# Optimization experiments

Hardware: AMD Instinct MI355X
Metric: run time of the kernel (lower is better)

## Reference

```python
import jax, jax.numpy as jnp
import numpy as np

N_NODES = 100000
N_EDGES = 1700000  # 1.6M random edges + 100k self-loops (dgl.add_self_loop)
HID = 128
N_GRAPHS = 64
N_CLASSES = 10
T_STEPS = 5


def setup_inputs() -> dict:
    key = jax.random.key(0)
    ks = jax.random.split(key, 12)
    m = jax.random.normal(ks[0], (N_NODES,), dtype=jnp.float32)
    n_rand = N_EDGES - N_NODES
    src_r = jax.random.randint(ks[1], (n_rand,), 0, N_NODES)
    dst_r = jax.random.randint(ks[2], (n_rand,), 0, N_NODES)
    loops = jnp.arange(N_NODES)
    src = jnp.concatenate([src_r, loops])
    dst = jnp.concatenate([dst_r, loops])
    graph_ids = jnp.sort(jax.random.randint(ks[3], (N_NODES,), 0, N_GRAPHS))
    s = 0.05
    W_e = jax.random.normal(ks[4], (HID, HID), dtype=jnp.float32) * s
    b_e = jnp.zeros((HID,), dtype=jnp.float32)
    W_ih = jax.random.normal(ks[5], (3 * HID, HID), dtype=jnp.float32) * s
    b_ih = jnp.zeros((3 * HID,), dtype=jnp.float32)
    W_hh = jax.random.normal(ks[6], (3 * HID, HID), dtype=jnp.float32) * s
    b_hh = jnp.zeros((3 * HID,), dtype=jnp.float32)
    W_cls = jax.random.normal(ks[7], (N_CLASSES, HID), dtype=jnp.float32) * s
    b_cls = jnp.zeros((N_CLASSES,), dtype=jnp.float32)
    return {"m": m, "W_e": W_e, "b_e": b_e, "W_ih": W_ih, "b_ih": b_ih,
            "W_hh": W_hh, "b_hh": b_hh, "W_cls": W_cls, "b_cls": b_cls,
            "src": src, "dst": dst, "graph_ids": graph_ids, "n_graphs": N_GRAPHS}


def _gated_graph_forward(m, W_e, b_e, W_ih, b_ih, W_hh, b_hh, W_cls, b_cls,
                         src, dst, graph_ids, n_graphs):
    n_nodes = m.shape[0]
    hid = W_e.shape[0]
    # h = ndata['m'].view(-1,1), zero-padded to out_feats (DGL GatedGraphConv)
    h = jnp.zeros((n_nodes, hid), dtype=m.dtype).at[:, 0].set(m)
    for _ in range(T_STEPS):
        # single edge type: a[v] = sum_{(u,v) in E} W_e h[u] + b_e
        msg = (h @ W_e.T + b_e)[src]                       # [E, H]
        a = jax.ops.segment_sum(msg, dst, num_segments=n_nodes)
        # torch.nn.GRUCell(a, h); gate order: r, z, n
        gi = a @ W_ih.T + b_ih
        gh = h @ W_hh.T + b_hh
        i_r, i_z, i_n = jnp.split(gi, 3, axis=-1)
        h_r, h_z, h_n = jnp.split(gh, 3, axis=-1)
        r = jax.nn.sigmoid(i_r + h_r)
        z = jax.nn.sigmoid(i_z + h_z)
        n = jnp.tanh(i_n + r * h_n)
        h = (1.0 - z) * n + z * h
    h = jax.nn.relu(h)
    # dgl.mean_nodes: per-graph mean over nodes
    sums = jax.ops.segment_sum(h, graph_ids, num_segments=n_graphs)
    cnt = jax.ops.segment_sum(jnp.ones((n_nodes,), h.dtype), graph_ids,
                              num_segments=n_graphs)
    hg = sums / jnp.maximum(cnt, 1.0)[:, None]             # [G, H]
    return hg @ W_cls.T + b_cls                            # [G, C]


def reference(m, W_e, b_e, W_ih, b_ih, W_hh, b_hh, W_cls, b_cls,
              src, dst, graph_ids, n_graphs):
    return _gated_graph_forward(m, W_e, b_e, W_ih, b_ih, W_hh, b_hh,
                                W_cls, b_cls, src, dst, graph_ids, n_graphs)
```

## Files before the change

### kernel.cpp

```cpp
#include <hip/hip_runtime.h>

#define HID 128
#define G3  384
#define TSTEPS 5
#define BSHIFT 9
#define BNODES (1 << BSHIFT)
#define MAXBUK 256
#define PART_EPB 8192

typedef unsigned int  uint;
typedef unsigned short ushort;

typedef float  f32x4  __attribute__((ext_vector_type(4)));
typedef __bf16 bf16x8 __attribute__((ext_vector_type(8)));

union B8u { uint4 u; bf16x8 b; ushort s[8]; };

static __device__ inline ushort f2bf(float f) {
  uint u = __float_as_uint(f);
  uint r = u + 0x7fffu + ((u >> 16) & 1u);
  return (ushort)(r >> 16);
}
static __device__ inline float bf2f(ushort s) {
  return __uint_as_float(((uint)s) << 16);
}

__global__ __launch_bounds__(128) void k_weights(
    const float* __restrict__ W_e, const float* __restrict__ b_e,
    const float* __restrict__ W_ih, const float* __restrict__ W_hh,
    ushort* __restrict__ Wcomb, ushort* __restrict__ Whh16, float* __restrict__ bvec,
    ushort* __restrict__ Wc0, ushort* __restrict__ Wh0)
{
  int j = blockIdx.x, t = threadIdx.x;
  if (j < G3) {
    __shared__ float row[HID];
    row[t] = W_ih[j * HID + t];
    __syncthreads();
    float acc = 0.f;
    for (int k = 0; k < HID; ++k) acc = fmaf(row[k], W_e[k * HID + t], acc);
    Wcomb[j * HID + t] = f2bf(acc);
    if (t == 0) {
      Wc0[j] = f2bf(acc);
      float b = 0.f;
      for (int k = 0; k < HID; ++k) b += row[k] * b_e[k];
      bvec[j] = b;
    }
  } else {
    int j2 = j - G3;
    Whh16[j2 * HID + t] = f2bf(W_hh[j2 * HID + t]);
    if (t == 0) Wh0[j2] = f2bf(W_hh[j2 * HID]);
  }
}

__global__ __launch_bounds__(256) void k_bh(const int* __restrict__ dst,
                                            int* __restrict__ bhist, int E) {
  __shared__ int lh[MAXBUK];
  int t = threadIdx.x;
  if (t < MAXBUK) lh[t] = 0;
  __syncthreads();
  for (int e = blockIdx.x * 256 + t; e < E; e += gridDim.x * 256)
    atomicAdd(&lh[dst[e] >> BSHIFT], 1);
  __syncthreads();
  if (t < MAXBUK && lh[t]) atomicAdd(&bhist[t], lh[t]);
}

__global__ __launch_bounds__(256) void k_bsc(const int* __restrict__ bhist,
                                             int* __restrict__ bbase,
                                             int* __restrict__ gcur,
                                             int* __restrict__ rowptr, int E, int N) {
  __shared__ int ls[MAXBUK];
  int t = threadIdx.x;
  ls[t] = bhist[t];
  __syncthreads();
  if (t == 0) {
    int run = 0;
    for (int i = 0; i < MAXBUK; ++i) {
      bbase[i] = run; gcur[i] = run; run += ls[i];
    }
    bbase[MAXBUK] = run;
    rowptr[N] = E;
  }
}

__global__ __launch_bounds__(256) void k_part(
    const int* __restrict__ src, const int* __restrict__ dst,
    int* __restrict__ gcur, uint* __restrict__ ebuf, int E) {
  __shared__ int lh[MAXBUK], lbase[MAXBUK], lcur[MAXBUK];
  int t = threadIdx.x;
  int base = blockIdx.x * PART_EPB;
  if (t < MAXBUK) lh[t] = 0;
  __syncthreads();
#pragma unroll 4
  for (int j = 0; j < PART_EPB / 256; ++j) {
    int e = base + j * 256 + t;
    if (e < E) atomicAdd(&lh[dst[e] >> BSHIFT], 1);
  }
  __syncthreads();
  if (t < MAXBUK) {
    lbase[t] = lh[t] ? atomicAdd(&gcur[t], lh[t]) : 0;
    lcur[t] = 0;
  }
  __syncthreads();
#pragma unroll 4
  for (int j = 0; j < PART_EPB / 256; ++j) {
    int e = base + j * 256 + t;
    if (e < E) {
      int d = dst[e];
      int b = d >> BSHIFT;
      int p = atomicAdd(&lcur[b], 1);
      ebuf[lbase[b] + p] = (uint)src[e] | ((uint)(d & (BNODES - 1)) << 20);
    }
  }
}

__global__ __launch_bounds__(256) void k_fill2(
    const uint* __restrict__ ebuf, const int* __restrict__ bbase,
    int* __restrict__ csrc, int* __restrict__ rowptr, int* __restrict__ deg, int N) {
  __shared__ int hcnt[BNODES];
  __shared__ int wls[4];
  int t = threadIdx.x;
  int b = blockIdx.x;
  int ebeg = bbase[b], eend = bbase[b + 1];
  for (int i = t; i < BNODES; i += 256) hcnt[i] = 0;
  __syncthreads();
  for (int e = ebeg + t; e < eend; e += 256)
    atomicAdd(&hcnt[ebuf[e] >> 20], 1);
  __syncthreads();
  const int PER = BNODES / 256;
  int lane = t & 63, wv = t >> 6;
  int x[PER]; int s = 0;
#pragma unroll
  for (int i = 0; i < PER; ++i) { x[i] = hcnt[PER * t + i]; s += x[i]; }
  int incl = s;
#pragma unroll
  for (int off = 1; off < 64; off <<= 1) {
    int u = __shfl_up(incl, off, 64);
    if (lane >= off) incl += u;
  }
  if (lane == 63) wls[wv] = incl;
  __syncthreads();
  int wbase = 0;
  for (int i = 0; i < wv; ++i) wbase += wls[i];
  int run = wbase + incl - s;
#pragma unroll
  for (int i = 0; i < PER; ++i) {
    int node = (b << BSHIFT) + PER * t + i;
    hcnt[PER * t + i] = run;
    if (node < N) { rowptr[node] = ebeg + run; deg[node] = x[i]; }
    run += x[i];
  }
  __syncthreads();
  for (int e = ebeg + t; e < eend; e += 256) {
    uint v = ebuf[e];
    int p = atomicAdd(&hcnt[v >> 20], 1);
    csrc[ebeg + p] = (int)(v & 0xFFFFFu);
  }
}

__global__ void k_minit(const float* __restrict__ m, ushort* __restrict__ m16, int N) {
  int v = blockIdx.x * 256 + threadIdx.x;
  if (v < N) m16[v] = f2bf(m[v]);
}

__global__ __launch_bounds__(256) void k_gather0(
    const int* __restrict__ rowptr, const int* __restrict__ csrc,
    const ushort* __restrict__ m16, ushort* __restrict__ hsum0, int N)
{
  int v = blockIdx.x * 256 + threadIdx.x;
  if (v >= N) return;
  int beg = rowptr[v], end = rowptr[v + 1];
  float a0 = 0.f, a1 = 0.f, a2 = 0.f, a3 = 0.f;
  int e = beg;
  for (; e + 16 <= end; e += 16) {
    a0 += (bf2f(m16[csrc[e + 0]]) + bf2f(m16[csrc[e + 4]])) +
          (bf2f(m16[csrc[e + 8]]) + bf2f(m16[csrc[e + 12]]));
    a1 += (bf2f(m16[csrc[e + 1]]) + bf2f(m16[csrc[e + 5]])) +
          (bf2f(m16[csrc[e + 9]]) + bf2f(m16[csrc[e + 13]]));
    a2 += (bf2f(m16[csrc[e + 2]]) + bf2f(m16[csrc[e + 6]])) +
          (bf2f(m16[csrc[e + 10]]) + bf2f(m16[csrc[e + 14]]));
    a3 += (bf2f(m16[csrc[e + 3]]) + bf2f(m16[csrc[e + 7]])) +
          (bf2f(m16[csrc[e + 11]]) + bf2f(m16[csrc[e + 15]]));
  }
  for (; e < end; e += 4) {
    if (e + 0 < end) a0 += bf2f(m16[csrc[e + 0]]);
    if (e + 1 < end) a1 += bf2f(m16[csrc[e + 1]]);
    if (e + 2 < end) a2 += bf2f(m16[csrc[e + 2]]);
    if (e + 3 < end) a3 += bf2f(m16[csrc[e + 3]]);
  }
  hsum0[v] = f2bf((a0 + a1) + (a2 + a3));
}

__global__ __launch_bounds__(256) void k_gru0(
    const ushort* __restrict__ hsum0, const ushort* __restrict__ m16,
    const int* __restrict__ deg,
    const ushort* __restrict__ Wc0, const ushort* __restrict__ Wh0,
    const float* __restrict__ bvec, const float* __restrict__ b_ih,
    const float* __restrict__ b_hh, ushort* __restrict__ hbn, int N)
{
  int idx = blockIdx.x * 256 + threadIdx.x;
  if (idx >= N * HID) return;
  int n = idx >> 7, d = idx & (HID - 1);
  float s0 = bf2f(hsum0[n]);
  float h0 = bf2f(m16[n]);
  float degf = (float)deg[n];
  float acc0 = s0 * bf2f(Wc0[d]);
  float acc1 = s0 * bf2f(Wc0[d + 128]);
  float acc2 = s0 * bf2f(Wc0[d + 256]);
  float acc3 = h0 * bf2f(Wh0[d]);
  float acc4 = h0 * bf2f(Wh0[d + 128]);
  float acc5 = h0 * bf2f(Wh0[d + 256]);
  float hold = (d == 0) ? h0 : 0.f;
  float ir = acc0 + degf * bvec[d] + b_ih[d];
  float iz = acc1 + degf * bvec[d + 128] + b_ih[d + 128];
  float in_ = acc2 + degf * bvec[d + 256] + b_ih[d + 256];
  float hr = acc3 + b_hh[d];
  float hz = acc4 + b_hh[d + 128];
  float hn = acc5 + b_hh[d + 256];
  float r = __builtin_amdgcn_rcpf(1.f + __expf(-(ir + hr)));
  float z = __builtin_amdgcn_rcpf(1.f + __expf(-(iz + hz)));
  float x2 = in_ + r * hn;
  float e2 = __expf(2.f * x2);
  float nv = 1.f - 2.f * __builtin_amdgcn_rcpf(e2 + 1.f);
  float hv = (1.f - z) * nv + z * hold;
  hbn[idx] = f2bf(hv);
}

__global__ __launch_bounds__(256) void k_gather(
    const int* __restrict__ rowptr, const int* __restrict__ csrc,
    const ushort* __restrict__ hb, ushort* __restrict__ hs16, int N, int nstrip)
{
  int x = blockIdx.x & 7;
  int ii = blockIdx.x >> 3;
  int s = 8 * (ii >> 2) + x;
  if (s >= nstrip) return;
  int v = s * 16 + (ii & 3) * 4 + (threadIdx.x >> 6);
  if (v >= N) return;
  int lane = threadIdx.x & 63;
  int g = lane >> 4;
  int i = lane & 15;
  int beg = rowptr[v], end = rowptr[v + 1];
  float acc[8] = {0.f, 0.f, 0.f, 0.f, 0.f, 0.f, 0.f, 0.f};
  int e = beg;
  for (; e + 16 <= end; e += 16) {
    int s0 = csrc[e + g];
    int s1 = csrc[e + 4 + g];
    int s2 = csrc[e + 8 + g];
    int s3 = csrc[e + 12 + g];
    B8u w0; w0.u = *(const uint4*)(hb + (size_t)s0 * HID + i * 8);
    B8u w1; w1.u = *(const uint4*)(hb + (size_t)s1 * HID + i * 8);
    B8u w2; w2.u = *(const uint4*)(hb + (size_t)s2 * HID + i * 8);
    B8u w3; w3.u = *(const uint4*)(hb + (size_t)s3 * HID + i * 8);
#pragma unroll
    for (int j = 0; j < 8; ++j)
      acc[j] += (bf2f(w0.s[j]) + bf2f(w1.s[j])) + (bf2f(w2.s[j]) + bf2f(w3.s[j]));
  }
  for (; e < end; e += 4) {
    int ee = e + g;
    if (ee < end) {
      int s0 = csrc[ee];
      B8u w; w.u = *(const uint4*)(hb + (size_t)s0 * HID + i * 8);
#pragma unroll
      for (int j = 0; j < 8; ++j) acc[j] += bf2f(w.s[j]);
    }
  }
#pragma unroll
  for (int j = 0; j < 8; ++j) {
    acc[j] += __shfl_xor(acc[j], 16, 64);
    acc[j] += __shfl_xor(acc[j], 32, 64);
  }
  if (g == 0) {
    uint4 ov;
    ov.x = ((uint)f2bf(acc[1]) << 16) | (uint)f2bf(acc[0]);
    ov.y = ((uint)f2bf(acc[3]) << 16) | (uint)f2bf(acc[2]);
    ov.z = ((uint)f2bf(acc[5]) << 16) | (uint)f2bf(acc[4]);
    ov.w = ((uint)f2bf(acc[7]) << 16) | (uint)f2bf(acc[6]);
    *(uint4*)(hs16 + (size_t)v * HID + i * 8) = ov;
  }
}

struct GruCtx2 {
  const ushort* Amat;
  const ushort* hbc; ushort* hbn; const int* deg;
  int l16, quad, gm3, d0, ecol, erow0;
  float bir, biz, bin_, bhr, bhz, bhn, vr, vz, vn;
};

static __device__ __forceinline__ void gru2_loadA(const GruCtx2& c, int s, B8u a[4]) {
  size_t arow = (size_t)(s * 16 + c.l16) * HID + c.quad * 8;
#pragma unroll
  for (int kc = 0; kc < 4; ++kc)
    a[kc].u = *(const uint4*)(c.Amat + arow + kc * 32);
}

static __device__ __forceinline__ void gru2_loadE(const GruCtx2& c, int s,
                                                  float hold[2], float dg[2]) {
  int n0 = s << 4;
  hold[0] = bf2f(c.hbc[(size_t)(n0 + c.erow0) * HID + c.ecol]);
  hold[1] = bf2f(c.hbc[(size_t)(n0 + c.erow0 + 8) * HID + c.ecol]);
  dg[0] = (float)c.deg[n0 + c.erow0];
  dg[1] = (float)c.deg[n0 + c.erow0 + 8];
}

static __device__ __forceinline__ void gru2_step(
    const GruCtx2& c, int s, const B8u a[4], const float hold[2], const float dg[2],
    const B8u bfr[3][4], float (*S)[16][132]) {
  f32x4 acc[3] = {};
#pragma unroll
  for (int kc = 0; kc < 4; ++kc)
#pragma unroll
    for (int g = 0; g < 3; ++g)
      acc[g] = __builtin_amdgcn_mfma_f32_16x16x32_bf16(a[kc].b, bfr[g][kc].b, acc[g], 0, 0, 0);
  __builtin_amdgcn_s_barrier();
#pragma unroll
  for (int g = 0; g < 3; ++g)
#pragma unroll
    for (int rg = 0; rg < 4; ++rg)
      S[c.gm3 + g][c.quad * 4 + rg][c.d0 + c.l16] = acc[g][rg];
  asm volatile("s_waitcnt lgkmcnt(0)" ::: "memory");
  __builtin_amdgcn_sched_barrier(0);
  __builtin_amdgcn_s_barrier();
  int n0 = s << 4;
#pragma unroll
  for (int k = 0; k < 2; ++k) {
    int row = c.erow0 + 8 * k;
    float ir  = S[0][row][c.ecol] + dg[k] * c.vr + c.bir;
    float iz  = S[1][row][c.ecol] + dg[k] * c.vz + c.biz;
    float in_ = S[2][row][c.ecol] + dg[k] * c.vn + c.bin_;
    float hr  = S[3][row][c.ecol] + c.bhr;
    float hz  = S[4][row][c.ecol] + c.bhz;
    float hn  = S[5][row][c.ecol] + c.bhn;
    float r = __builtin_amdgcn_rcpf(1.f + __expf(-(ir + hr)));
    float z = __builtin_amdgcn_rcpf(1.f + __expf(-(iz + hz)));
    float x2 = in_ + r * hn;
    float e2 = __expf(2.f * x2);
    float nv = 1.f - 2.f * __builtin_amdgcn_rcpf(e2 + 1.f);
    float hv = (1.f - z) * nv + z * hold[k];
    c.hbn[(size_t)(n0 + row) * HID + c.ecol] = f2bf(hv);
  }
}

__global__ __launch_bounds__(1024, 4) void k_gru(
    const ushort* __restrict__ hs16,
    const ushort* __restrict__ hbc, ushort* __restrict__ hbn,
    const ushort* __restrict__ Wcomb, const ushort* __restrict__ Whh16,
    const float* __restrict__ bvec, const float* __restrict__ b_ih,
    const float* __restrict__ b_hh, const int* __restrict__ deg, int N)
{
  __shared__ float S[6][16][132];
  const int tid = threadIdx.x;
  const int w = tid >> 6;
  const int lane = tid & 63;
  const int quad = lane >> 4, l16 = lane & 15;
  const int gm = w >> 3;
  const int gw = w & 7;
  const int d0 = gw * 16;

  const ushort* Wmat = gm ? Whh16 : Wcomb;

  B8u bfr[3][4];
#pragma unroll
  for (int g = 0; g < 3; ++g)
#pragma unroll
    for (int kc = 0; kc < 4; ++kc) {
      int j = (d0 + g * 128 + l16) * HID + kc * 32 + quad * 8;
      bfr[g][kc].u = *(const uint4*)(Wmat + j);
    }

  GruCtx2 c;
  c.Amat = gm ? hbc : hs16;
  c.hbc = hbc; c.hbn = hbn; c.deg = deg;
  c.l16 = l16; c.quad = quad; c.gm3 = gm * 3; c.d0 = d0;
  c.ecol = tid & 127;
  c.erow0 = tid >> 7;
  c.bir = b_ih[c.ecol]; c.biz = b_ih[c.ecol + 128]; c.bin_ = b_ih[c.ecol + 256];
  c.bhr = b_hh[c.ecol]; c.bhz = b_hh[c.ecol + 128]; c.bhn = b_hh[c.ecol + 256];
  c.vr = bvec[c.ecol]; c.vz = bvec[c.ecol + 128]; c.vn = bvec[c.ecol + 256];

  const int nstrip = N >> 4;
  const int G = (int)gridDim.x;
  int s = blockIdx.x;
  if (s >= nstrip) return;

  B8u aA[4], aB[4];
  float hA[2], dA[2], hB[2], dB[2];
  gru2_loadA(c, s, aA); gru2_loadE(c, s, hA, dA);

  while (true) {
    int ns = s + G;
    bool more = ns < nstrip;
    if (more) { gru2_loadA(c, ns, aB); gru2_loadE(c, ns, hB, dB); }
    gru2_step(c, s, aA, hA, dA, bfr, S);
    if (!more) break;
    s = ns;
    ns = s + G;
    more = ns < nstrip;
    if (more) { gru2_loadA(c, ns, aA); gru2_loadE(c, ns, hA, dA); }
    gru2_step(c, s, aB, hB, dB, bfr, S);
    if (!more) break;
    s = ns;
  }
}

__global__ __launch_bounds__(64) void k_bounds(const int* __restrict__ gid,
                                               int* __restrict__ cnt, int N, int G) {
  int g = threadIdx.x;
  if (g >= G) return;
  int lo = 0, hi = N;
  while (lo < hi) { int mid = (lo + hi) >> 1; if (gid[mid] < g) lo = mid + 1; else hi = mid; }
  int lb0 = lo;
  lo = 0; hi = N;
  int g1 = g + 1;
  while (lo < hi) { int mid = (lo + hi) >> 1; if (gid[mid] < g1) lo = mid + 1; else hi = mid; }
  cnt[g] = lo - lb0;
}

#define POOL_CHUNK 96
__global__ __launch_bounds__(128) void k_pool(const ushort* __restrict__ hb,
                                              const int* __restrict__ gid,
                                              float* __restrict__ hg, int N) {
  int d = threadIdx.x;
  int start = blockIdx.x * POOL_CHUNK;
  if (start >= N) return;
  int end = min(start + POOL_CHUNK, N);
  float acc = 0.f;
  int g = gid[start];
  for (int n = start; n < end; ++n) {
    int gn = gid[n];
    if (gn != g) { unsafeAtomicAdd(&hg[g * HID + d], acc); acc = 0.f; g = gn; }
    acc += fmaxf(bf2f(hb[(size_t)n * HID + d]), 0.f);
  }
  unsafeAtomicAdd(&hg[g * HID + d], acc);
}

__global__ __launch_bounds__(640) void k_cls(const float* __restrict__ hg,
                                             const int* __restrict__ cnt,
                                             const float* __restrict__ Wc,
                                             const float* __restrict__ bc,
                                             float* __restrict__ out, int G) {
  int t = threadIdx.x;
  if (t >= G * 10) return;
  int g = t / 10, c = t % 10;
  float inv = 1.f / fmaxf((float)cnt[g], 1.f);
  float acc = 0.f;
  for (int d = 0; d < HID; ++d) acc = fmaf(hg[g * HID + d], Wc[c * HID + d], acc);
  out[t] = acc * inv + bc[c];
}

extern "C" void kernel_launch(void* const* d_in, const int* in_sizes, int n_in,
                              void* d_out, int out_size, void* d_ws, size_t ws_size,
                              hipStream_t stream) {
  const int N = in_sizes[0];
  const int E = in_sizes[9];
  const float* m    = (const float*)d_in[0];
  const float* W_e  = (const float*)d_in[1];
  const float* b_e  = (const float*)d_in[2];
  const float* W_ih = (const float*)d_in[3];
  const float* b_ih = (const float*)d_in[4];
  const float* W_hh = (const float*)d_in[5];
  const float* b_hh = (const float*)d_in[6];
  const float* W_cls = (const float*)d_in[7];
  const float* b_cls = (const float*)d_in[8];
  const int* src = (const int*)d_in[9];
  const int* dst = (const int*)d_in[10];
  const int* gid = (const int*)d_in[11];
  const int G = out_size / 10;
  float* out = (float*)d_out;

  size_t off = 0;
  auto alloc = [&](size_t b) {
    char* p = (char*)d_ws + off;
    off += (b + 255) & ~(size_t)255;
    return (void*)p;
  };
  ushort* hb0    = (ushort*)alloc((size_t)N * HID * 2);
  ushort* hb1    = (ushort*)alloc((size_t)N * HID * 2);
  ushort* hs16   = (ushort*)alloc((size_t)N * HID * 2);
  int*    deg    = (int*)   alloc((size_t)N * 4);
  int*    rowptr = (int*)   alloc((size_t)(N + 1) * 4);
  int*    csrc   = (int*)   alloc((size_t)E * 4);
  uint*   ebuf   = (uint*)  alloc((size_t)E * 4);
  int*    bhist  = (int*)   alloc((size_t)MAXBUK * 4);
  int*    bbase  = (int*)   alloc((size_t)(MAXBUK + 1) * 4);
  int*    gcur   = (int*)   alloc((size_t)MAXBUK * 4);
  ushort* Wcomb  = (ushort*)alloc((size_t)G3 * HID * 2);
  ushort* Whh16  = (ushort*)alloc((size_t)G3 * HID * 2);
  float*  bvec   = (float*) alloc((size_t)G3 * 4);
  float*  hg     = (float*) alloc((size_t)G * HID * 4);
  int*    cnt    = (int*)   alloc((size_t)G * 4);
  ushort* m16    = (ushort*)alloc((size_t)N * 2);
  ushort* hsum0  = (ushort*)alloc((size_t)N * 2);
  ushort* Wc0    = (ushort*)alloc((size_t)G3 * 2);
  ushort* Wh0    = (ushort*)alloc((size_t)G3 * 2);
  if (off > ws_size) return;

  const int NBUK = (N + BNODES - 1) >> BSHIFT;

  k_weights<<<2 * G3, HID, 0, stream>>>(W_e, b_e, W_ih, W_hh, Wcomb, Whh16, bvec, Wc0, Wh0);
  k_minit<<<(N + 255) / 256, 256, 0, stream>>>(m, m16, N);
  hipMemsetAsync(bhist, 0, (size_t)MAXBUK * 4, stream);
  k_bh<<<256, 256, 0, stream>>>(dst, bhist, E);
  k_bsc<<<1, MAXBUK, 0, stream>>>(bhist, bbase, gcur, rowptr, E, N);
  k_part<<<(E + PART_EPB - 1) / PART_EPB, 256, 0, stream>>>(src, dst, gcur, ebuf, E);
  k_fill2<<<NBUK, 256, 0, stream>>>(ebuf, bbase, csrc, rowptr, deg, N);

  k_gather0<<<(N + 255) / 256, 256, 0, stream>>>(rowptr, csrc, m16, hsum0, N);
  k_gru0<<<(N * HID + 255) / 256, 256, 0, stream>>>(hsum0, m16, deg, Wc0, Wh0,
                                                    bvec, b_ih, b_hh, hb1, N);

  ushort* hbc = hb1;
  ushort* hbn = hb0;
  const int nstrip = N >> 4;
  const int gather_blocks = 8 * ((nstrip + 7) / 8) * 4;
  const int gru_blocks = nstrip < 256 ? nstrip : 256;
  for (int s = 1; s < TSTEPS; ++s) {
    k_gather<<<gather_blocks, 256, 0, stream>>>(rowptr, csrc, hbc, hs16, N, nstrip);
    k_gru<<<gru_blocks, 1024, 0, stream>>>(hs16, hbc, hbn, Wcomb, Whh16, bvec, b_ih, b_hh, deg, N);
    ushort* t = hbc; hbc = hbn; hbn = t;
  }

  hipMemsetAsync(hg, 0, (size_t)G * HID * 4, stream);
  k_bounds<<<1, 64, 0, stream>>>(gid, cnt, N, G);
  k_pool<<<(N + POOL_CHUNK - 1) / POOL_CHUNK, HID, 0, stream>>>(hbc, gid, hg, N);
  k_cls<<<1, 640, 0, stream>>>(hg, cnt, W_cls, b_cls, out, G);
}
```

Measured before the change: 812.0 us.

## Fuse neighbor gather into GRU kernel with triple-buffered LDS strips

Merges the per-step gather kernel and the GRU MFMA kernel into one persistent kernel. Each 16-wave block gathers the neighbor sums and old hidden rows for the next 16-node strip directly into swizzled LDS while computing the current strip, so the hs16 intermediate is never written to or read back from global memory. The cost is that gather work now runs at only 256 blocks with one wave per node, which gives less latency hiding for the random-access gather than the previous wide launch. It also uses more LDS per block.

```diff
diff --git a/kernel.cpp b/kernel.cpp
--- a/kernel.cpp
+++ b/kernel.cpp
@@ -225,20 +225,21 @@
   hbn[idx] = f2bf(hv);
 }
 
-__global__ __launch_bounds__(256) void k_gather(
+static __device__ __forceinline__ void gather_strip(
     const int* __restrict__ rowptr, const int* __restrict__ csrc,
-    const ushort* __restrict__ hb, ushort* __restrict__ hs16, int N, int nstrip)
+    const ushort* __restrict__ hb, const int* __restrict__ deg,
+    int strip, int w, int lane, int N,
+    ushort dstS[16][128], ushort dstH[16][128], int* dstDeg)
 {
-  int x = blockIdx.x & 7;
-  int ii = blockIdx.x >> 3;
-  int s = 8 * (ii >> 2) + x;
-  if (s >= nstrip) return;
-  int v = s * 16 + (ii & 3) * 4 + (threadIdx.x >> 6);
-  if (v >= N) return;
-  int lane = threadIdx.x & 63;
+  int node = strip * 16 + w;
+  if (node >= N) return;
   int g = lane >> 4;
   int i = lane & 15;
-  int beg = rowptr[v], end = rowptr[v + 1];
+  if (g == 1)
+    *(uint4*)(&dstH[w][(i ^ (w & 7)) * 8]) =
+        *(const uint4*)(hb + (size_t)node * HID + i * 8);
+  if (lane == 32) dstDeg[w] = deg[node];
+  int beg = rowptr[node], end = rowptr[node + 1];
   float acc[8] = {0.f, 0.f, 0.f, 0.f, 0.f, 0.f, 0.f, 0.f};
   int e = beg;
   for (; e + 16 <= end; e += 16) {
@@ -258,9 +259,9 @@
     int ee = e + g;
     if (ee < end) {
       int s0 = csrc[ee];
-      B8u w; w.u = *(const uint4*)(hb + (size_t)s0 * HID + i * 8);
-#pragma unroll
-      for (int j = 0; j < 8; ++j) acc[j] += bf2f(w.s[j]);
+      B8u wv; wv.u = *(const uint4*)(hb + (size_t)s0 * HID + i * 8);
+#pragma unroll
+      for (int j = 0; j < 8; ++j) acc[j] += bf2f(wv.s[j]);
     }
   }
 #pragma unroll
@@ -274,79 +275,20 @@
     ov.y = ((uint)f2bf(acc[3]) << 16) | (uint)f2bf(acc[2]);
     ov.z = ((uint)f2bf(acc[5]) << 16) | (uint)f2bf(acc[4]);
     ov.w = ((uint)f2bf(acc[7]) << 16) | (uint)f2bf(acc[6]);
-    *(uint4*)(hs16 + (size_t)v * HID + i * 8) = ov;
-  }
-}
-
-struct GruCtx2 {
-  const ushort* Amat;
-  const ushort* hbc; ushort* hbn; const int* deg;
-  int l16, quad, gm3, d0, ecol, erow0;
-  float bir, biz, bin_, bhr, bhz, bhn, vr, vz, vn;
-};
-
-static __device__ __forceinline__ void gru2_loadA(const GruCtx2& c, int s, B8u a[4]) {
-  size_t arow = (size_t)(s * 16 + c.l16) * HID + c.quad * 8;
-#pragma unroll
-  for (int kc = 0; kc < 4; ++kc)
-    a[kc].u = *(const uint4*)(c.Amat + arow + kc * 32);
-}
-
-static __device__ __forceinline__ void gru2_loadE(const GruCtx2& c, int s,
-                                                  float hold[2], float dg[2]) {
-  int n0 = s << 4;
-  hold[0] = bf2f(c.hbc[(size_t)(n0 + c.erow0) * HID + c.ecol]);
-  hold[1] = bf2f(c.hbc[(size_t)(n0 + c.erow0 + 8) * HID + c.ecol]);
-  dg[0] = (float)c.deg[n0 + c.erow0];
-  dg[1] = (float)c.deg[n0 + c.erow0 + 8];
-}
-
-static __device__ __forceinline__ void gru2_step(
-    const GruCtx2& c, int s, const B8u a[4], const float hold[2], const float dg[2],
-    const B8u bfr[3][4], float (*S)[16][132]) {
-  f32x4 acc[3] = {};
-#pragma unroll
-  for (int kc = 0; kc < 4; ++kc)
-#pragma unroll
-    for (int g = 0; g < 3; ++g)
-      acc[g] = __builtin_amdgcn_mfma_f32_16x16x32_bf16(a[kc].b, bfr[g][kc].b, acc[g], 0, 0, 0);
-  __builtin_amdgcn_s_barrier();
-#pragma unroll
-  for (int g = 0; g < 3; ++g)
-#pragma unroll
-    for (int rg = 0; rg < 4; ++rg)
-      S[c.gm3 + g][c.quad * 4 + rg][c.d0 + c.l16] = acc[g][rg];
-  asm volatile("s_waitcnt lgkmcnt(0)" ::: "memory");
-  __builtin_amdgcn_sched_barrier(0);
-  __builtin_amdgcn_s_barrier();
-  int n0 = s << 4;
-#pragma unroll
-  for (int k = 0; k < 2; ++k) {
-    int row = c.erow0 + 8 * k;
-    float ir  = S[0][row][c.ecol] + dg[k] * c.vr + c.bir;
-    float iz  = S[1][row][c.ecol] + dg[k] * c.vz + c.biz;
-    float in_ = S[2][row][c.ecol] + dg[k] * c.vn + c.bin_;
-    float hr  = S[3][row][c.ecol] + c.bhr;
-    float hz  = S[4][row][c.ecol] + c.bhz;
-    float hn  = S[5][row][c.ecol] + c.bhn;
-    float r = __builtin_amdgcn_rcpf(1.f + __expf(-(ir + hr)));
-    float z = __builtin_amdgcn_rcpf(1.f + __expf(-(iz + hz)));
-    float x2 = in_ + r * hn;
-    float e2 = __expf(2.f * x2);
-    float nv = 1.f - 2.f * __builtin_amdgcn_rcpf(e2 + 1.f);
-    float hv = (1.f - z) * nv + z * hold[k];
-    c.hbn[(size_t)(n0 + row) * HID + c.ecol] = f2bf(hv);
-  }
-}
-
-__global__ __launch_bounds__(1024, 4) void k_gru(
-    const ushort* __restrict__ hs16,
+    *(uint4*)(&dstS[w][(i ^ (w & 7)) * 8]) = ov;
+  }
+}
+
+__global__ __launch_bounds__(1024, 4) void k_fused(
+    const int* __restrict__ rowptr, const int* __restrict__ csrc,
     const ushort* __restrict__ hbc, ushort* __restrict__ hbn,
     const ushort* __restrict__ Wcomb, const ushort* __restrict__ Whh16,
     const float* __restrict__ bvec, const float* __restrict__ b_ih,
     const float* __restrict__ b_hh, const int* __restrict__ deg, int N)
 {
   __shared__ float S[6][16][132];
+  __shared__ ushort AT[3][2][16][128];
+  __shared__ int degT[3][16];
   const int tid = threadIdx.x;
   const int w = tid >> 6;
   const int lane = tid & 63;
@@ -356,7 +298,6 @@
   const int d0 = gw * 16;
 
   const ushort* Wmat = gm ? Whh16 : Wcomb;
-
   B8u bfr[3][4];
 #pragma unroll
   for (int g = 0; g < 3; ++g)
@@ -366,38 +307,71 @@
       bfr[g][kc].u = *(const uint4*)(Wmat + j);
     }
 
-  GruCtx2 c;
-  c.Amat = gm ? hbc : hs16;
-  c.hbc = hbc; c.hbn = hbn; c.deg = deg;
-  c.l16 = l16; c.quad = quad; c.gm3 = gm * 3; c.d0 = d0;
-  c.ecol = tid & 127;
-  c.erow0 = tid >> 7;
-  c.bir = b_ih[c.ecol]; c.biz = b_ih[c.ecol + 128]; c.bin_ = b_ih[c.ecol + 256];
-  c.bhr = b_hh[c.ecol]; c.bhz = b_hh[c.ecol + 128]; c.bhn = b_hh[c.ecol + 256];
-  c.vr = bvec[c.ecol]; c.vz = bvec[c.ecol + 128]; c.vn = bvec[c.ecol + 256];
+  const int ecol = tid & 127, erow0 = tid >> 7;
+  const float bir = b_ih[ecol], biz = b_ih[ecol + 128], bin_ = b_ih[ecol + 256];
+  const float bhr = b_hh[ecol], bhz = b_hh[ecol + 128], bhn = b_hh[ecol + 256];
+  const float vr = bvec[ecol], vz = bvec[ecol + 128], vn = bvec[ecol + 256];
 
   const int nstrip = N >> 4;
   const int G = (int)gridDim.x;
   int s = blockIdx.x;
   if (s >= nstrip) return;
 
-  B8u aA[4], aB[4];
-  float hA[2], dA[2], hB[2], dB[2];
-  gru2_loadA(c, s, aA); gru2_loadE(c, s, hA, dA);
-
+  gather_strip(rowptr, csrc, hbc, deg, s, w, lane, N, AT[0][0], AT[0][1], degT[0]);
+  asm volatile("s_waitcnt lgkmcnt(0)" ::: "memory");
+  __builtin_amdgcn_sched_barrier(0);
+  __builtin_amdgcn_s_barrier();
+
+  int cur = 0;
   while (true) {
     int ns = s + G;
     bool more = ns < nstrip;
-    if (more) { gru2_loadA(c, ns, aB); gru2_loadE(c, ns, hB, dB); }
-    gru2_step(c, s, aA, hA, dA, bfr, S);
+    int nxt = (cur == 2) ? 0 : cur + 1;
+    if (more)
+      gather_strip(rowptr, csrc, hbc, deg, ns, w, lane, N,
+                   AT[nxt][0], AT[nxt][1], degT[nxt]);
+    B8u af[4];
+#pragma unroll
+    for (int kc = 0; kc < 4; ++kc)
+      af[kc].u = *(const uint4*)(&AT[cur][gm][l16][(((quad + 4 * kc) ^ (l16 & 7)) * 8)]);
+    f32x4 acc[3] = {};
+#pragma unroll
+    for (int kc = 0; kc < 4; ++kc)
+#pragma unroll
+      for (int g = 0; g < 3; ++g)
+        acc[g] = __builtin_amdgcn_mfma_f32_16x16x32_bf16(af[kc].b, bfr[g][kc].b, acc[g], 0, 0, 0);
+    __builtin_amdgcn_s_barrier();
+#pragma unroll
+    for (int g = 0; g < 3; ++g)
+#pragma unroll
+      for (int rg = 0; rg < 4; ++rg)
+        S[gm * 3 + g][quad * 4 + rg][d0 + l16] = acc[g][rg];
+    asm volatile("s_waitcnt lgkmcnt(0)" ::: "memory");
+    __builtin_amdgcn_sched_barrier(0);
+    __builtin_amdgcn_s_barrier();
+    int n0 = s << 4;
+#pragma unroll
+    for (int k = 0; k < 2; ++k) {
+      int row = erow0 + 8 * k;
+      float dgf = (float)degT[cur][row];
+      int sc = (((ecol >> 3) ^ (row & 7)) * 8) + (ecol & 7);
+      float hold = bf2f(AT[cur][1][row][sc]);
+      float ir  = S[0][row][ecol] + dgf * vr + bir;
+      float iz  = S[1][row][ecol] + dgf * vz + biz;
+      float in_ = S[2][row][ecol] + dgf * vn + bin_;
+      float hr  = S[3][row][ecol] + bhr;
+      float hz  = S[4][row][ecol] + bhz;
+      float hn  = S[5][row][ecol] + bhn;
+      float r = __builtin_amdgcn_rcpf(1.f + __expf(-(ir + hr)));
+      float z = __builtin_amdgcn_rcpf(1.f + __expf(-(iz + hz)));
+      float x2 = in_ + r * hn;
+      float e2 = __expf(2.f * x2);
+      float nv = 1.f - 2.f * __builtin_amdgcn_rcpf(e2 + 1.f);
+      float hv = (1.f - z) * nv + z * hold;
+      hbn[(size_t)(n0 + row) * HID + ecol] = f2bf(hv);
+    }
     if (!more) break;
-    s = ns;
-    ns = s + G;
-    more = ns < nstrip;
-    if (more) { gru2_loadA(c, ns, aA); gru2_loadE(c, ns, hA, dA); }
-    gru2_step(c, s, aB, hB, dB, bfr, S);
-    if (!more) break;
-    s = ns;
+    s = ns; cur = nxt;
   }
 }
 
@@ -474,7 +448,6 @@
   };
   ushort* hb0    = (ushort*)alloc((size_t)N * HID * 2);
   ushort* hb1    = (ushort*)alloc((size_t)N * HID * 2);
-  ushort* hs16   = (ushort*)alloc((size_t)N * HID * 2);
   int*    deg    = (int*)   alloc((size_t)N * 4);
   int*    rowptr = (int*)   alloc((size_t)(N + 1) * 4);
   int*    csrc   = (int*)   alloc((size_t)E * 4);
@@ -510,11 +483,10 @@
   ushort* hbc = hb1;
   ushort* hbn = hb0;
   const int nstrip = N >> 4;
-  const int gather_blocks = 8 * ((nstrip + 7) / 8) * 4;
-  const int gru_blocks = nstrip < 256 ? nstrip : 256;
+  const int fuse_blocks = nstrip < 256 ? nstrip : 256;
   for (int s = 1; s < TSTEPS; ++s) {
-    k_gather<<<gather_blocks, 256, 0, stream>>>(rowptr, csrc, hbc, hs16, N, nstrip);
-    k_gru<<<gru_blocks, 1024, 0, stream>>>(hs16, hbc, hbn, Wcomb, Whh16, bvec, b_ih, b_hh, deg, N);
+    k_fused<<<fuse_blocks, 1024, 0, stream>>>(rowptr, csrc, hbc, hbn,
+                                              Wcomb, Whh16, bvec, b_ih, b_hh, deg, N);
     ushort* t = hbc; hbc = hbn; hbn = t;
   }
 
```

Result: faster. 795.5 us (-2.0%).
